# Kernel optimization log

Measured on AMD Instinct MI355X. Metric: run time of the kernel, lower is better.

## Reference

```python
import jax, jax.numpy as jnp
import numpy as np

B, L, S, H, E, D = 4, 2048, 2048, 8, 64, 64

def setup_inputs() -> dict:
    key = jax.random.key(0)
    kq, kk, kv = jax.random.split(key, 3)
    queries = jax.random.normal(kq, (B, L, H, E), dtype=jnp.float32)
    keys = jax.random.normal(kk, (B, S, H, E), dtype=jnp.float32)
    values = jax.random.normal(kv, (B, S, H, D), dtype=jnp.float32)
    return {"queries": queries, "keys": keys, "values": values}

def reference(queries, keys, values):
    # scale = self.scale or 1/sqrt(E)
    scale = 1.0 / jnp.sqrt(jnp.float32(queries.shape[-1]))
    # scores: [B, H, L, S]
    scores = jnp.einsum('blhe,bshe->bhls', queries, keys)
    # dropout is identity at inference (Keras Dropout only active in training)
    A = jax.nn.softmax(scale * scores, axis=-1)
    # output: [B, L, H, D]
    return jnp.einsum('bhls,bshd->blhd', A, values)
```

## Files before the change

kernel.cpp:

```cpp
#include <hip/hip_runtime.h>


#define B_ 4
#define L_ 2048
#define S_ 2048
#define H_ 8

#define NUMSZ (B_ * L_ * H_ * 64)
#define LSZ (B_ * L_ * H_)
#define KVELEM (B_ * H_ * S_ * 64)
#define TILE_ELEMS 2048

typedef __attribute__((ext_vector_type(8))) __bf16 bf16x8;
typedef __attribute__((ext_vector_type(4))) __bf16 bf16x4;
typedef __attribute__((ext_vector_type(16))) float floatx16;

union BF4U { bf16x4 v; uint2 u; };
union BF8U { bf16x8 v; uint4 u; };

__device__ __forceinline__ void async_load16(const void* g, void* l) {
  __builtin_amdgcn_global_load_lds(
      (const __attribute__((address_space(1))) unsigned int*)g,
      (__attribute__((address_space(3))) unsigned int*)l, 16, 0, 0);
}

__device__ __forceinline__ bf16x8 cvt8(float4 a, float4 b) {
  bf16x8 r;
  r[0] = (__bf16)a.x; r[1] = (__bf16)a.y; r[2] = (__bf16)a.z; r[3] = (__bf16)a.w;
  r[4] = (__bf16)b.x; r[5] = (__bf16)b.y; r[6] = (__bf16)b.z; r[7] = (__bf16)b.w;
  return r;
}

__device__ __forceinline__ void softmax_pb(const floatx16& sc, int h32, float& l,
                                           bf16x8& pB0v, bf16x8& pB1v) {
  BF4U pg[4];
#pragma unroll
  for (int g = 0; g < 4; ++g) {
    float p0 = __builtin_amdgcn_exp2f(sc[4 * g + 0]);
    float p1 = __builtin_amdgcn_exp2f(sc[4 * g + 1]);
    float p2 = __builtin_amdgcn_exp2f(sc[4 * g + 2]);
    float p3 = __builtin_amdgcn_exp2f(sc[4 * g + 3]);
    l += (p0 + p1) + (p2 + p3);
    pg[g].v = (bf16x4){(__bf16)p0, (__bf16)p1, (__bf16)p2, (__bf16)p3};
  }
  uint2 sendA = h32 ? pg[0].u : pg[1].u;
  uint2 sendB = h32 ? pg[2].u : pg[3].u;
  uint2 recvA, recvB;
  recvA.x = __shfl_xor((int)sendA.x, 32);
  recvA.y = __shfl_xor((int)sendA.y, 32);
  recvB.x = __shfl_xor((int)sendB.x, 32);
  recvB.y = __shfl_xor((int)sendB.y, 32);
  BF8U pB0, pB1;
  if (h32 == 0) {
    pB0.u = (uint4){pg[0].u.x, pg[0].u.y, recvA.x, recvA.y};
    pB1.u = (uint4){pg[2].u.x, pg[2].u.y, recvB.x, recvB.y};
  } else {
    pB0.u = (uint4){recvA.x, recvA.y, pg[1].u.x, pg[1].u.y};
    pB1.u = (uint4){recvB.x, recvB.y, pg[3].u.x, pg[3].u.y};
  }
  pB0v = pB0.v;
  pB1v = pB1.v;
}

__global__ __launch_bounds__(256) void prep_kernel(const float* __restrict__ K,
                                                   const float* __restrict__ V,
                                                   __bf16* __restrict__ Kb,
                                                   __bf16* __restrict__ Vb) {
  __shared__ float Vs[32 * 64];
  const int bid = blockIdx.x;
  const int xcd = bid & 7;
  const int idx = bid >> 3;
  const int pair = xcd * 4 + (idx >> 6);
  const int tile = idx & 63;
  const int h = pair & 7;
  const int b = pair >> 3;
  const int obid = pair * 64 + tile;
  const int s0 = tile * 32;
  const int i = threadIdx.x;

  {
    const int s = i >> 3, cp = i & 7;
    const int e0 = 8 * (cp ^ (s & 7));
    const float* src = K + (((size_t)(b * S_ + s0 + s) * H_ + h) * 64 + e0);
    float4 a = *(const float4*)src;
    float4 bb = *(const float4*)(src + 4);
    *(bf16x8*)(Kb + (size_t)obid * TILE_ELEMS + i * 8) = cvt8(a, bb);
  }
  {
    const int s = i >> 3, d0 = (i & 7) * 8;
    const float* src = V + (((size_t)(b * S_ + s0 + s) * H_ + h) * 64 + d0);
    float4 a = *(const float4*)src;
    float4 bb = *(const float4*)(src + 4);
    *(float4*)&Vs[s * 64 + d0] = a;
    *(float4*)&Vs[s * 64 + d0 + 4] = bb;
  }
  __syncthreads();
  {
    const int Ll = i >> 3, cp = i & 7;
    const int ci = cp ^ (Ll & 7);
    const int d = 2 * Ll + (ci >> 2);
    const int ch = ci & 3;
    BF8U o;
#pragma unroll
    for (int j = 0; j < 8; ++j) o.v[j] = (__bf16)Vs[(8 * ch + j) * 64 + d];
    *(bf16x8*)(Vb + (size_t)obid * TILE_ELEMS + i * 8) = o.v;
  }
}

__global__ __launch_bounds__(256, 3) void attn_kernel(const float* __restrict__ Q,
                                                      const __bf16* __restrict__ Kb,
                                                      const __bf16* __restrict__ Vb,
                                                      float* __restrict__ O,
                                                      float* __restrict__ num_ws,
                                                      float* __restrict__ l_ws,
                                                      int splits) {
  __shared__ __align__(16) __bf16 Kt[2][2 * TILE_ELEMS];
  __shared__ __align__(16) __bf16 Vt[2][2 * TILE_ELEMS];

  const int tid = threadIdx.x;
  const int lane = tid & 63;
  const int wave = tid >> 6;
  const int q32 = lane & 31;
  const int h32 = lane >> 5;

  const int bid = blockIdx.x;
  const int xcd = bid & 7;
  const int idx = bid >> 3;
  const int bs = 16 * splits;
  const int pairl = idx / bs;
  const int sub = idx - pairl * bs;
  const int pair = xcd * 4 + pairl;
  const int qb = sub & 15;
  const int split = sub >> 4;
  const int h = pair & 7;
  const int b = pair >> 3;

  int nt2, tile0;
  if (splits == 3) {
    nt2 = (split < 2) ? 11 : 10;
    tile0 = 22 * split;
  } else {
    nt2 = (S_ / 32) / (2 * splits);
    tile0 = split * 2 * nt2;
  }

  const float qscale = 0.125f * 1.44269504088896340736f;
  const int qrow = qb * 128 + wave * 32 + q32;
  bf16x8 qf[4];
  {
    const float* qp = Q + ((size_t)(b * L_ + qrow) * H_ + h) * 64;
#pragma unroll
    for (int c = 0; c < 4; ++c) {
      const float* p = qp + c * 16 + h32 * 8;
      float4 a = *(const float4*)p;
      float4 bb = *(const float4*)(p + 4);
      float t[8] = {a.x, a.y, a.z, a.w, bb.x, bb.y, bb.z, bb.w};
#pragma unroll
      for (int j = 0; j < 8; ++j) qf[c][j] = (__bf16)(t[j] * qscale);
    }
  }

  int koff[4];
#pragma unroll
  for (int c = 0; c < 4; ++c) koff[c] = (q32 * 8 + (((2 * c + h32) ^ (q32 & 7)))) * 8;
  int voff[2][2];
#pragma unroll
  for (int s2 = 0; s2 < 2; ++s2)
#pragma unroll
    for (int dt = 0; dt < 2; ++dt) {
      int dp = dt * 32 + q32;
      int Ll = dp >> 1;
      int ci = (dp & 1) * 4 + 2 * s2 + h32;
      voff[s2][dt] = (Ll * 8 + (ci ^ (Ll & 7))) * 8;
    }

  float l = 0.f;
  floatx16 ot[2];
#pragma unroll
  for (int r = 0; r < 16; ++r) { ot[0][r] = 0.f; ot[1][r] = 0.f; }

  const __bf16* KbBH = Kb + (size_t)(pair * 64) * TILE_ELEMS;
  const __bf16* VbBH = Vb + (size_t)(pair * 64) * TILE_ELEMS;
  const int lin8 = (wave * 64 + lane) * 8;

#pragma unroll
  for (int st = 0; st < 2; ++st) {
    async_load16(KbBH + (size_t)(tile0 + st) * TILE_ELEMS + lin8,
                 &Kt[0][st * TILE_ELEMS + wave * 512]);
    async_load16(VbBH + (size_t)(tile0 + st) * TILE_ELEMS + lin8,
                 &Vt[0][st * TILE_ELEMS + wave * 512]);
  }

  for (int t = 0; t < nt2; ++t) {
    const int buf = t & 1;
    __syncthreads();

    if (t + 1 < nt2) {
#pragma unroll
      for (int st = 0; st < 2; ++st) {
        async_load16(KbBH + (size_t)(tile0 + 2 * (t + 1) + st) * TILE_ELEMS + lin8,
                     &Kt[buf ^ 1][st * TILE_ELEMS + wave * 512]);
        async_load16(VbBH + (size_t)(tile0 + 2 * (t + 1) + st) * TILE_ELEMS + lin8,
                     &Vt[buf ^ 1][st * TILE_ELEMS + wave * 512]);
      }
    }

    const __bf16* Kbuf0 = &Kt[buf][0];
    const __bf16* Kbuf1 = &Kt[buf][TILE_ELEMS];
    const __bf16* Vbuf0 = &Vt[buf][0];
    const __bf16* Vbuf1 = &Vt[buf][TILE_ELEMS];

    floatx16 sc0;
#pragma unroll
    for (int r = 0; r < 16; ++r) sc0[r] = 0.f;
    {
      bf16x8 kA0[4];
#pragma unroll
      for (int c = 0; c < 4; ++c) kA0[c] = *(const bf16x8*)&Kbuf0[koff[c]];
      __builtin_amdgcn_s_setprio(1);
#pragma unroll
      for (int c = 0; c < 4; ++c)
        sc0 = __builtin_amdgcn_mfma_f32_32x32x16_bf16(kA0[c], qf[c], sc0, 0, 0, 0);
      __builtin_amdgcn_s_setprio(0);
    }
    floatx16 sc1;
#pragma unroll
    for (int r = 0; r < 16; ++r) sc1[r] = 0.f;
    {
      bf16x8 kA1[4];
#pragma unroll
      for (int c = 0; c < 4; ++c) kA1[c] = *(const bf16x8*)&Kbuf1[koff[c]];
      __builtin_amdgcn_s_setprio(1);
#pragma unroll
      for (int c = 0; c < 4; ++c)
        sc1 = __builtin_amdgcn_mfma_f32_32x32x16_bf16(kA1[c], qf[c], sc1, 0, 0, 0);
      __builtin_amdgcn_s_setprio(0);
    }

    bf16x8 p00, p01;
    softmax_pb(sc0, h32, l, p00, p01);

    {
      bf16x8 vA0[4];
      vA0[0] = *(const bf16x8*)&Vbuf0[voff[0][0]];
      vA0[1] = *(const bf16x8*)&Vbuf0[voff[0][1]];
      vA0[2] = *(const bf16x8*)&Vbuf0[voff[1][0]];
      vA0[3] = *(const bf16x8*)&Vbuf0[voff[1][1]];
      __builtin_amdgcn_s_setprio(1);
      ot[0] = __builtin_amdgcn_mfma_f32_32x32x16_bf16(vA0[0], p00, ot[0], 0, 0, 0);
      ot[1] = __builtin_amdgcn_mfma_f32_32x32x16_bf16(vA0[1], p00, ot[1], 0, 0, 0);
      ot[0] = __builtin_amdgcn_mfma_f32_32x32x16_bf16(vA0[2], p01, ot[0], 0, 0, 0);
      ot[1] = __builtin_amdgcn_mfma_f32_32x32x16_bf16(vA0[3], p01, ot[1], 0, 0, 0);
      __builtin_amdgcn_s_setprio(0);
    }

    bf16x8 p10, p11;
    softmax_pb(sc1, h32, l, p10, p11);

    {
      bf16x8 vA1[4];
      vA1[0] = *(const bf16x8*)&Vbuf1[voff[0][0]];
      vA1[1] = *(const bf16x8*)&Vbuf1[voff[0][1]];
      vA1[2] = *(const bf16x8*)&Vbuf1[voff[1][0]];
      vA1[3] = *(const bf16x8*)&Vbuf1[voff[1][1]];
      __builtin_amdgcn_s_setprio(1);
      ot[0] = __builtin_amdgcn_mfma_f32_32x32x16_bf16(vA1[0], p10, ot[0], 0, 0, 0);
      ot[1] = __builtin_amdgcn_mfma_f32_32x32x16_bf16(vA1[1], p10, ot[1], 0, 0, 0);
      ot[0] = __builtin_amdgcn_mfma_f32_32x32x16_bf16(vA1[2], p11, ot[0], 0, 0, 0);
      ot[1] = __builtin_amdgcn_mfma_f32_32x32x16_bf16(vA1[3], p11, ot[1], 0, 0, 0);
      __builtin_amdgcn_s_setprio(0);
    }
  }

  {
    float lg = l + __shfl_xor(l, 32);
    if (splits == 1) {
      const float inv = 1.0f / lg;
      float* orow = O + ((size_t)(b * L_ + qrow) * H_ + h) * 64;
#pragma unroll
      for (int dt = 0; dt < 2; ++dt)
#pragma unroll
        for (int gg = 0; gg < 4; ++gg) {
          float4 v = {ot[dt][4 * gg + 0] * inv, ot[dt][4 * gg + 1] * inv,
                      ot[dt][4 * gg + 2] * inv, ot[dt][4 * gg + 3] * inv};
          *(float4*)(orow + dt * 32 + gg * 8 + h32 * 4) = v;
        }
    } else {
      float* nrow =
          num_ws + (size_t)split * NUMSZ + ((size_t)(b * L_ + qrow) * H_ + h) * 64;
#pragma unroll
      for (int dt = 0; dt < 2; ++dt)
#pragma unroll
        for (int gg = 0; gg < 4; ++gg) {
          float4 v = {ot[dt][4 * gg + 0], ot[dt][4 * gg + 1],
                      ot[dt][4 * gg + 2], ot[dt][4 * gg + 3]};
          *(float4*)(nrow + dt * 32 + gg * 8 + h32 * 4) = v;
        }
      if (h32 == 0)
        l_ws[(size_t)split * LSZ + (size_t)(b * L_ + qrow) * H_ + h] = lg;
    }
  }
}

__global__ __launch_bounds__(256) void combine_kernel(const float* __restrict__ num_ws,
                                                      const float* __restrict__ l_ws,
                                                      float* __restrict__ O, int splits) {
  const size_t i4 = ((size_t)blockIdx.x * 256 + threadIdx.x) * 4;
  float4 acc = {0.f, 0.f, 0.f, 0.f};
  float lt = 0.f;
  for (int s = 0; s < splits; ++s) {
    float4 v = *(const float4*)(num_ws + (size_t)s * NUMSZ + i4);
    acc.x += v.x; acc.y += v.y; acc.z += v.z; acc.w += v.w;
    lt += l_ws[(size_t)s * LSZ + (i4 >> 6)];
  }
  const float inv = 1.0f / lt;
  float4 o = {acc.x * inv, acc.y * inv, acc.z * inv, acc.w * inv};
  *(float4*)(O + i4) = o;
}

extern "C" void kernel_launch(void* const* d_in, const int* in_sizes, int n_in,
                              void* d_out, int out_size, void* d_ws, size_t ws_size,
                              hipStream_t stream) {
  const float* Q = (const float*)d_in[0];
  const float* K = (const float*)d_in[1];
  const float* V = (const float*)d_in[2];
  float* O = (float*)d_out;

  __bf16* Kb = (__bf16*)d_ws;
  __bf16* Vb = Kb + KVELEM;
  float* num_ws = (float*)(Vb + KVELEM);
  const size_t base = (size_t)2 * KVELEM * sizeof(__bf16);
  const size_t per_split = ((size_t)NUMSZ + (size_t)LSZ) * sizeof(float);
  int splits = 1;
  if (ws_size >= base + 3 * per_split) splits = 3;
  else if (ws_size >= base + 2 * per_split) splits = 2;
  float* l_ws = num_ws + (size_t)splits * NUMSZ;

  prep_kernel<<<B_ * H_ * 64, 256, 0, stream>>>(K, V, Kb, Vb);
  dim3 grid(B_ * H_ * 16 * splits);
  attn_kernel<<<grid, 256, 0, stream>>>(Q, Kb, Vb, O, num_ws, l_ws, splits);
  if (splits > 1) {
    combine_kernel<<<NUMSZ / 4 / 256, 256, 0, stream>>>(num_ws, l_ws, O, splits);
  }
}
```

Before: 148.0 us.

## Triple-buffer K/V tiles with partial vmcnt waits instead of full sync

Expands the shared K/V staging from two to three buffers and issues loads two iterations ahead. Replaces __syncthreads with an s_waitcnt vmcnt that waits only for the current stage's loads, followed by a raw s_barrier, so prefetches can stay in flight across the barrier. This raises LDS use per block, which could limit occupancy, and relies on hand-written wait counts matching the issued loads.

```diff
diff --git a/kernel.cpp b/kernel.cpp
--- a/kernel.cpp
+++ b/kernel.cpp
@@ -114,8 +114,8 @@
                                                       float* __restrict__ num_ws,
                                                       float* __restrict__ l_ws,
                                                       int splits) {
-  __shared__ __align__(16) __bf16 Kt[2][2 * TILE_ELEMS];
-  __shared__ __align__(16) __bf16 Vt[2][2 * TILE_ELEMS];
+  __shared__ __align__(16) __bf16 Kt[3][2 * TILE_ELEMS];
+  __shared__ __align__(16) __bf16 Vt[3][2 * TILE_ELEMS];
 
   const int tid = threadIdx.x;
   const int lane = tid & 63;
@@ -183,32 +183,36 @@
   const __bf16* VbBH = Vb + (size_t)(pair * 64) * TILE_ELEMS;
   const int lin8 = (wave * 64 + lane) * 8;
 
-#pragma unroll
-  for (int st = 0; st < 2; ++st) {
-    async_load16(KbBH + (size_t)(tile0 + st) * TILE_ELEMS + lin8,
-                 &Kt[0][st * TILE_ELEMS + wave * 512]);
-    async_load16(VbBH + (size_t)(tile0 + st) * TILE_ELEMS + lin8,
-                 &Vt[0][st * TILE_ELEMS + wave * 512]);
-  }
-
+  auto stage = [&](int bufi, int tp) {
+    async_load16(KbBH + (size_t)tp * TILE_ELEMS + lin8, &Kt[bufi][wave * 512]);
+    async_load16(KbBH + (size_t)(tp + 1) * TILE_ELEMS + lin8,
+                 &Kt[bufi][TILE_ELEMS + wave * 512]);
+    async_load16(VbBH + (size_t)tp * TILE_ELEMS + lin8, &Vt[bufi][wave * 512]);
+    async_load16(VbBH + (size_t)(tp + 1) * TILE_ELEMS + lin8,
+                 &Vt[bufi][TILE_ELEMS + wave * 512]);
+  };
+
+  stage(0, tile0);
+  if (nt2 > 1) stage(1, tile0 + 2);
+
+  int cur = 0;
   for (int t = 0; t < nt2; ++t) {
-    const int buf = t & 1;
-    __syncthreads();
-
     if (t + 1 < nt2) {
-#pragma unroll
-      for (int st = 0; st < 2; ++st) {
-        async_load16(KbBH + (size_t)(tile0 + 2 * (t + 1) + st) * TILE_ELEMS + lin8,
-                     &Kt[buf ^ 1][st * TILE_ELEMS + wave * 512]);
-        async_load16(VbBH + (size_t)(tile0 + 2 * (t + 1) + st) * TILE_ELEMS + lin8,
-                     &Vt[buf ^ 1][st * TILE_ELEMS + wave * 512]);
-      }
-    }
-
-    const __bf16* Kbuf0 = &Kt[buf][0];
-    const __bf16* Kbuf1 = &Kt[buf][TILE_ELEMS];
-    const __bf16* Vbuf0 = &Vt[buf][0];
-    const __bf16* Vbuf1 = &Vt[buf][TILE_ELEMS];
+      asm volatile("s_waitcnt vmcnt(4)" ::: "memory");
+    } else {
+      asm volatile("s_waitcnt vmcnt(0)" ::: "memory");
+    }
+    asm volatile("s_barrier" ::: "memory");
+
+    if (t + 2 < nt2) {
+      int nn = cur + 2; if (nn >= 3) nn -= 3;
+      stage(nn, tile0 + 2 * (t + 2));
+    }
+
+    const __bf16* Kbuf0 = &Kt[cur][0];
+    const __bf16* Kbuf1 = &Kt[cur][TILE_ELEMS];
+    const __bf16* Vbuf0 = &Vt[cur][0];
+    const __bf16* Vbuf1 = &Vt[cur][TILE_ELEMS];
 
     floatx16 sc0;
 #pragma unroll
@@ -239,7 +243,6 @@
 
     bf16x8 p00, p01;
     softmax_pb(sc0, h32, l, p00, p01);
-
     {
       bf16x8 vA0[4];
       vA0[0] = *(const bf16x8*)&Vbuf0[voff[0][0]];
@@ -256,7 +259,6 @@
 
     bf16x8 p10, p11;
     softmax_pb(sc1, h32, l, p10, p11);
-
     {
       bf16x8 vA1[4];
       vA1[0] = *(const bf16x8*)&Vbuf1[voff[0][0]];
@@ -270,6 +272,8 @@
       ot[1] = __builtin_amdgcn_mfma_f32_32x32x16_bf16(vA1[3], p11, ot[1], 0, 0, 0);
       __builtin_amdgcn_s_setprio(0);
     }
+
+    cur = (cur + 1 == 3) ? 0 : cur + 1;
   }
 
   {
```

Result: no change. 147.3 us (-0.5%).

## Load K/V MFMA fragments directly from global in register layout, drop LDS staging

Applied to the files above, without the earlier changes.

The prep kernel now writes K and V bf16 tiles in the exact per-lane MFMA operand order, so the attention kernel can read each wave's fragments with contiguous 16-byte global loads. This removes the LDS double buffer, the async global-to-LDS copies and the per-iteration block barrier. Each wave now fetches K/V separately through L2/L1 rather than sharing one LDS copy across four waves, and there is no explicit prefetch of the next tile. The maximum split count also drops from three to two, reducing the grid and the combine work.

```diff
diff --git a/kernel.cpp b/kernel.cpp
--- a/kernel.cpp
+++ b/kernel.cpp
@@ -17,12 +17,6 @@
 
 union BF4U { bf16x4 v; uint2 u; };
 union BF8U { bf16x8 v; uint4 u; };
-
-__device__ __forceinline__ void async_load16(const void* g, void* l) {
-  __builtin_amdgcn_global_load_lds(
-      (const __attribute__((address_space(1))) unsigned int*)g,
-      (__attribute__((address_space(3))) unsigned int*)l, 16, 0, 0);
-}
 
 __device__ __forceinline__ bf16x8 cvt8(float4 a, float4 b) {
   bf16x8 r;
@@ -77,11 +71,14 @@
   const int obid = pair * 64 + tile;
   const int s0 = tile * 32;
   const int i = threadIdx.x;
-
-  {
-    const int s = i >> 3, cp = i & 7;
-    const int e0 = 8 * (cp ^ (s & 7));
-    const float* src = K + (((size_t)(b * S_ + s0 + s) * H_ + h) * 64 + e0);
+  const int chunk = i >> 6;
+  const int l = i & 63;
+  const int q32 = l & 31;
+  const int h32 = l >> 5;
+
+  {
+    const float* src =
+        K + (((size_t)(b * S_ + s0 + q32) * H_ + h) * 64 + (2 * chunk + h32) * 8);
     float4 a = *(const float4*)src;
     float4 bb = *(const float4*)(src + 4);
     *(bf16x8*)(Kb + (size_t)obid * TILE_ELEMS + i * 8) = cvt8(a, bb);
@@ -96,13 +93,12 @@
   }
   __syncthreads();
   {
-    const int Ll = i >> 3, cp = i & 7;
-    const int ci = cp ^ (Ll & 7);
-    const int d = 2 * Ll + (ci >> 2);
-    const int ch = ci & 3;
+    const int s2 = chunk >> 1, dt = chunk & 1;
+    const int d = dt * 32 + q32;
+    const int sbase = 8 * (2 * s2 + h32);
     BF8U o;
 #pragma unroll
-    for (int j = 0; j < 8; ++j) o.v[j] = (__bf16)Vs[(8 * ch + j) * 64 + d];
+    for (int j = 0; j < 8; ++j) o.v[j] = (__bf16)Vs[(sbase + j) * 64 + d];
     *(bf16x8*)(Vb + (size_t)obid * TILE_ELEMS + i * 8) = o.v;
   }
 }
@@ -114,9 +110,6 @@
                                                       float* __restrict__ num_ws,
                                                       float* __restrict__ l_ws,
                                                       int splits) {
-  __shared__ __align__(16) __bf16 Kt[2][2 * TILE_ELEMS];
-  __shared__ __align__(16) __bf16 Vt[2][2 * TILE_ELEMS];
-
   const int tid = threadIdx.x;
   const int lane = tid & 63;
   const int wave = tid >> 6;
@@ -160,116 +153,66 @@
     }
   }
 
-  int koff[4];
-#pragma unroll
-  for (int c = 0; c < 4; ++c) koff[c] = (q32 * 8 + (((2 * c + h32) ^ (q32 & 7)))) * 8;
-  int voff[2][2];
-#pragma unroll
-  for (int s2 = 0; s2 < 2; ++s2)
-#pragma unroll
-    for (int dt = 0; dt < 2; ++dt) {
-      int dp = dt * 32 + q32;
-      int Ll = dp >> 1;
-      int ci = (dp & 1) * 4 + 2 * s2 + h32;
-      voff[s2][dt] = (Ll * 8 + (ci ^ (Ll & 7))) * 8;
-    }
-
   float l = 0.f;
   floatx16 ot[2];
 #pragma unroll
   for (int r = 0; r < 16; ++r) { ot[0][r] = 0.f; ot[1][r] = 0.f; }
 
-  const __bf16* KbBH = Kb + (size_t)(pair * 64) * TILE_ELEMS;
-  const __bf16* VbBH = Vb + (size_t)(pair * 64) * TILE_ELEMS;
-  const int lin8 = (wave * 64 + lane) * 8;
-
-#pragma unroll
-  for (int st = 0; st < 2; ++st) {
-    async_load16(KbBH + (size_t)(tile0 + st) * TILE_ELEMS + lin8,
-                 &Kt[0][st * TILE_ELEMS + wave * 512]);
-    async_load16(VbBH + (size_t)(tile0 + st) * TILE_ELEMS + lin8,
-                 &Vt[0][st * TILE_ELEMS + wave * 512]);
-  }
+  const __bf16* KbL = Kb + (size_t)(pair * 64) * TILE_ELEMS + lane * 8;
+  const __bf16* VbL = Vb + (size_t)(pair * 64) * TILE_ELEMS + lane * 8;
 
   for (int t = 0; t < nt2; ++t) {
-    const int buf = t & 1;
-    __syncthreads();
-
-    if (t + 1 < nt2) {
-#pragma unroll
-      for (int st = 0; st < 2; ++st) {
-        async_load16(KbBH + (size_t)(tile0 + 2 * (t + 1) + st) * TILE_ELEMS + lin8,
-                     &Kt[buf ^ 1][st * TILE_ELEMS + wave * 512]);
-        async_load16(VbBH + (size_t)(tile0 + 2 * (t + 1) + st) * TILE_ELEMS + lin8,
-                     &Vt[buf ^ 1][st * TILE_ELEMS + wave * 512]);
-      }
-    }
-
-    const __bf16* Kbuf0 = &Kt[buf][0];
-    const __bf16* Kbuf1 = &Kt[buf][TILE_ELEMS];
-    const __bf16* Vbuf0 = &Vt[buf][0];
-    const __bf16* Vbuf1 = &Vt[buf][TILE_ELEMS];
+    const size_t toff = (size_t)(tile0 + 2 * t) * TILE_ELEMS;
+    const __bf16* K0 = KbL + toff;
+    const __bf16* K1 = K0 + TILE_ELEMS;
+    const __bf16* V0 = VbL + toff;
+    const __bf16* V1 = V0 + TILE_ELEMS;
+
+    bf16x8 kA0[4], kA1[4], vA0[4], vA1[4];
+#pragma unroll
+    for (int c = 0; c < 4; ++c) kA0[c] = *(const bf16x8*)(K0 + c * 512);
+#pragma unroll
+    for (int c = 0; c < 4; ++c) kA1[c] = *(const bf16x8*)(K1 + c * 512);
+#pragma unroll
+    for (int c = 0; c < 4; ++c) vA0[c] = *(const bf16x8*)(V0 + c * 512);
+#pragma unroll
+    for (int c = 0; c < 4; ++c) vA1[c] = *(const bf16x8*)(V1 + c * 512);
 
     floatx16 sc0;
 #pragma unroll
     for (int r = 0; r < 16; ++r) sc0[r] = 0.f;
-    {
-      bf16x8 kA0[4];
-#pragma unroll
-      for (int c = 0; c < 4; ++c) kA0[c] = *(const bf16x8*)&Kbuf0[koff[c]];
-      __builtin_amdgcn_s_setprio(1);
-#pragma unroll
-      for (int c = 0; c < 4; ++c)
-        sc0 = __builtin_amdgcn_mfma_f32_32x32x16_bf16(kA0[c], qf[c], sc0, 0, 0, 0);
-      __builtin_amdgcn_s_setprio(0);
-    }
+    __builtin_amdgcn_s_setprio(1);
+#pragma unroll
+    for (int c = 0; c < 4; ++c)
+      sc0 = __builtin_amdgcn_mfma_f32_32x32x16_bf16(kA0[c], qf[c], sc0, 0, 0, 0);
+    __builtin_amdgcn_s_setprio(0);
+
     floatx16 sc1;
 #pragma unroll
     for (int r = 0; r < 16; ++r) sc1[r] = 0.f;
-    {
-      bf16x8 kA1[4];
-#pragma unroll
-      for (int c = 0; c < 4; ++c) kA1[c] = *(const bf16x8*)&Kbuf1[koff[c]];
-      __builtin_amdgcn_s_setprio(1);
-#pragma unroll
-      for (int c = 0; c < 4; ++c)
-        sc1 = __builtin_amdgcn_mfma_f32_32x32x16_bf16(kA1[c], qf[c], sc1, 0, 0, 0);
-      __builtin_amdgcn_s_setprio(0);
-    }
+    __builtin_amdgcn_s_setprio(1);
+#pragma unroll
+    for (int c = 0; c < 4; ++c)
+      sc1 = __builtin_amdgcn_mfma_f32_32x32x16_bf16(kA1[c], qf[c], sc1, 0, 0, 0);
+    __builtin_amdgcn_s_setprio(0);
 
     bf16x8 p00, p01;
     softmax_pb(sc0, h32, l, p00, p01);
-
-    {
-      bf16x8 vA0[4];
-      vA0[0] = *(const bf16x8*)&Vbuf0[voff[0][0]];
-      vA0[1] = *(const bf16x8*)&Vbuf0[voff[0][1]];
-      vA0[2] = *(const bf16x8*)&Vbuf0[voff[1][0]];
-      vA0[3] = *(const bf16x8*)&Vbuf0[voff[1][1]];
-      __builtin_amdgcn_s_setprio(1);
-      ot[0] = __builtin_amdgcn_mfma_f32_32x32x16_bf16(vA0[0], p00, ot[0], 0, 0, 0);
-      ot[1] = __builtin_amdgcn_mfma_f32_32x32x16_bf16(vA0[1], p00, ot[1], 0, 0, 0);
-      ot[0] = __builtin_amdgcn_mfma_f32_32x32x16_bf16(vA0[2], p01, ot[0], 0, 0, 0);
-      ot[1] = __builtin_amdgcn_mfma_f32_32x32x16_bf16(vA0[3], p01, ot[1], 0, 0, 0);
-      __builtin_amdgcn_s_setprio(0);
-    }
+    __builtin_amdgcn_s_setprio(1);
+    ot[0] = __builtin_amdgcn_mfma_f32_32x32x16_bf16(vA0[0], p00, ot[0], 0, 0, 0);
+    ot[1] = __builtin_amdgcn_mfma_f32_32x32x16_bf16(vA0[1], p00, ot[1], 0, 0, 0);
+    ot[0] = __builtin_amdgcn_mfma_f32_32x32x16_bf16(vA0[2], p01, ot[0], 0, 0, 0);
+    ot[1] = __builtin_amdgcn_mfma_f32_32x32x16_bf16(vA0[3], p01, ot[1], 0, 0, 0);
+    __builtin_amdgcn_s_setprio(0);
 
     bf16x8 p10, p11;
     softmax_pb(sc1, h32, l, p10, p11);
-
-    {
-      bf16x8 vA1[4];
-      vA1[0] = *(const bf16x8*)&Vbuf1[voff[0][0]];
-      vA1[1] = *(const bf16x8*)&Vbuf1[voff[0][1]];
-      vA1[2] = *(const bf16x8*)&Vbuf1[voff[1][0]];
-      vA1[3] = *(const bf16x8*)&Vbuf1[voff[1][1]];
-      __builtin_amdgcn_s_setprio(1);
-      ot[0] = __builtin_amdgcn_mfma_f32_32x32x16_bf16(vA1[0], p10, ot[0], 0, 0, 0);
-      ot[1] = __builtin_amdgcn_mfma_f32_32x32x16_bf16(vA1[1], p10, ot[1], 0, 0, 0);
-      ot[0] = __builtin_amdgcn_mfma_f32_32x32x16_bf16(vA1[2], p11, ot[0], 0, 0, 0);
-      ot[1] = __builtin_amdgcn_mfma_f32_32x32x16_bf16(vA1[3], p11, ot[1], 0, 0, 0);
-      __builtin_amdgcn_s_setprio(0);
-    }
+    __builtin_amdgcn_s_setprio(1);
+    ot[0] = __builtin_amdgcn_mfma_f32_32x32x16_bf16(vA1[0], p10, ot[0], 0, 0, 0);
+    ot[1] = __builtin_amdgcn_mfma_f32_32x32x16_bf16(vA1[1], p10, ot[1], 0, 0, 0);
+    ot[0] = __builtin_amdgcn_mfma_f32_32x32x16_bf16(vA1[2], p11, ot[0], 0, 0, 0);
+    ot[1] = __builtin_amdgcn_mfma_f32_32x32x16_bf16(vA1[3], p11, ot[1], 0, 0, 0);
+    __builtin_amdgcn_s_setprio(0);
   }
 
   {
@@ -332,8 +275,7 @@
   const size_t base = (size_t)2 * KVELEM * sizeof(__bf16);
   const size_t per_split = ((size_t)NUMSZ + (size_t)LSZ) * sizeof(float);
   int splits = 1;
-  if (ws_size >= base + 3 * per_split) splits = 3;
-  else if (ws_size >= base + 2 * per_split) splits = 2;
+  if (ws_size >= base + 2 * per_split) splits = 2;
   float* l_ws = num_ws + (size_t)splits * NUMSZ;
 
   prep_kernel<<<B_ * H_ * 64, 256, 0, stream>>>(K, V, Kb, Vb);
```

New measurement: 145.8 us. Within noise of the previous version (-1.5%).
